# Kernel tuning notes

Measured on AMD Instinct MI355X. Metric: run time of the kernel, lower is better.

Reference implementation:

```python
import jax, jax.numpy as jnp
import numpy as np

N_NODES = 400000
N_EDGES = 800000
N_GRAPHS = 16384
IN_DIM = 78
GNN_DIMS = [128, 128, 128]
FF_DIMS = [256, 128]


def _glorot(key, shape):
    fan_in, fan_out = shape
    lim = np.sqrt(6.0 / (fan_in + fan_out))
    return jax.random.uniform(key, shape, jnp.float32, -lim, lim)


def setup_inputs() -> dict:
    key = jax.random.key(0)
    ks = jax.random.split(key, 16)
    x = jax.random.normal(ks[0], (N_NODES, IN_DIM), jnp.float32)
    edge_index = jax.random.randint(ks[1], (2, N_EDGES), 0, N_NODES, jnp.int64)
    batch = jnp.sort(jax.random.randint(ks[2], (N_NODES,), 0, N_GRAPHS, jnp.int64))
    d = dict(x=x, edge_index=edge_index, batch=batch, n_graphs=N_GRAPHS)
    dims = [IN_DIM] + GNN_DIMS
    for i in range(3):
        d[f'gW{i}'] = _glorot(ks[3 + i], (dims[i], dims[i + 1]))
        d[f'gb{i}'] = jnp.zeros((dims[i + 1],), jnp.float32)
    fdims = [GNN_DIMS[-1]] + FF_DIMS
    for i in range(2):
        d[f'fW{i}'] = _glorot(ks[8 + i], (fdims[i], fdims[i + 1]))
        d[f'fb{i}'] = jnp.zeros((fdims[i + 1],), jnp.float32)
    return d


def gcn_conv(x, src, dst, deg_isqrt, W, b, n_nodes):
    # GCNConv: linear first, then propagate with sym norm over A + I
    h = x @ W  # [N, D]
    norm = (deg_isqrt[src] * deg_isqrt[dst])[:, None]  # [E, 1]
    msg = h[src] * norm  # [E, D] gather
    out = jax.ops.segment_sum(msg, dst, num_segments=n_nodes)  # scatter-add
    # self-loop contribution: norm_ii = deg_i^-1
    out = out + h * (deg_isqrt * deg_isqrt)[:, None]
    return out + b


def reference(x, edge_index, batch, n_graphs,
              gW0, gb0, gW1, gb1, gW2, gb2,
              fW0, fb0, fW1, fb1):
    n_nodes = x.shape[0]
    src, dst = edge_index[0], edge_index[1]
    # degree of A + I on target side
    deg = 1.0 + jax.ops.segment_sum(jnp.ones((src.shape[0],), x.dtype), dst,
                                    num_segments=n_nodes)
    deg_isqrt = jax.lax.rsqrt(deg)
    for W, b in ((gW0, gb0), (gW1, gb1), (gW2, gb2)):
        x = jax.nn.relu(gcn_conv(x, src, dst, deg_isqrt, W, b, n_nodes))
    # global max pool per graph (empty segments -> 0; x >= 0 post-ReLU)
    pooled = jax.ops.segment_max(x, batch, num_segments=n_graphs)
    pooled = jnp.where(jnp.isfinite(pooled), pooled, 0.0)
    # FF head: Linear -> ReLU -> Dropout(eval: identity)
    h = jax.nn.relu(pooled @ fW0 + fb0)
    h = jax.nn.relu(h @ fW1 + fb1)
    return h
```

## Files before the change

### kernel.cpp

```cpp
#include <hip/hip_runtime.h>

#define NN 400000
#define NE 800000
#define NG 16384

typedef short bf16x8 __attribute__((ext_vector_type(8)));
typedef float f32x4 __attribute__((ext_vector_type(4)));
typedef unsigned short u16x8 __attribute__((ext_vector_type(8)));

static inline int cdiv(int a, int b) { return (a + b - 1) / b; }

__device__ inline unsigned short bf16_rne(float v) {
    unsigned u = __float_as_uint(v);
    unsigned r = u + 0x7FFFu + ((u >> 16) & 1u);
    return (unsigned short)(r >> 16);
}
__device__ inline float bf16_to_f(unsigned short h) {
    return __uint_as_float(((unsigned)h) << 16);
}
__device__ inline void split2(float v, unsigned short& hi, unsigned short& lo) {
    hi = bf16_rne(v);
    lo = bf16_rne(v - bf16_to_f(hi));
}

__global__ __launch_bounds__(256) void fill_kernel(float* __restrict__ p, float v, int n) {
    int i = blockIdx.x * blockDim.x + threadIdx.x;
    if (i < n) p[i] = v;
}

__global__ __launch_bounds__(256) void fill_int_kernel(int* __restrict__ p, int v, int n) {
    int i = blockIdx.x * blockDim.x + threadIdx.x;
    if (i < n) p[i] = v;
}

__global__ __launch_bounds__(256) void hist_kernel(const int* __restrict__ dst,
                                                   int* __restrict__ deg, int E) {
    int e = blockIdx.x * blockDim.x + threadIdx.x;
    if (e < E) atomicAdd(&deg[dst[e]], 1);
}

__global__ __launch_bounds__(256) void disq_kernel(const int* __restrict__ deg,
                                                   float* __restrict__ disq, int n) {
    int i = blockIdx.x * blockDim.x + threadIdx.x;
    if (i < n) disq[i] = rsqrtf(1.0f + (float)deg[i]);
}

#define SCAN_TPB 256
#define SCAN_EPT 8
#define SCAN_BE (SCAN_TPB * SCAN_EPT)

__global__ __launch_bounds__(SCAN_TPB) void scan_a_kernel(const int* __restrict__ in,
                                                          int* __restrict__ out,
                                                          int* __restrict__ partials, int n) {
    __shared__ int sums[SCAN_TPB];
    const int tid = threadIdx.x;
    int base = blockIdx.x * SCAN_BE + tid * SCAN_EPT;
    int v[SCAN_EPT];
    int s = 0;
#pragma unroll
    for (int i = 0; i < SCAN_EPT; ++i) {
        int idx = base + i;
        int x = (idx < n) ? in[idx] : 0;
        v[i] = s;
        s += x;
    }
    sums[tid] = s;
    __syncthreads();
    for (int off = 1; off < SCAN_TPB; off <<= 1) {
        int t = (tid >= off) ? sums[tid - off] : 0;
        __syncthreads();
        sums[tid] += t;
        __syncthreads();
    }
    int toff = (tid == 0) ? 0 : sums[tid - 1];
#pragma unroll
    for (int i = 0; i < SCAN_EPT; ++i) {
        int idx = base + i;
        if (idx < n) out[idx] = toff + v[i];
    }
    if (tid == SCAN_TPB - 1) partials[blockIdx.x] = sums[SCAN_TPB - 1];
}

__global__ void scan_b_kernel(int* __restrict__ partials, int nb) {
    if (blockIdx.x == 0 && threadIdx.x == 0) {
        int s = 0;
        for (int i = 0; i < nb; ++i) { int x = partials[i]; partials[i] = s; s += x; }
    }
}

__global__ __launch_bounds__(256) void scan_c_kernel(int* __restrict__ out,
                                                     const int* __restrict__ partials, int n) {
    int idx = blockIdx.x * blockDim.x + threadIdx.x;
    if (idx < n) out[idx] += partials[idx / SCAN_BE];
}

__global__ __launch_bounds__(256) void csr_fill_kernel(const int* __restrict__ src,
                                                       const int* __restrict__ dst,
                                                       const int* __restrict__ rowptr,
                                                       int* __restrict__ cnt,
                                                       const float* __restrict__ disq,
                                                       int2* __restrict__ csr_ent, int E) {
    int e = blockIdx.x * blockDim.x + threadIdx.x;
    if (e >= E) return;
    int d = dst[e], s = src[e];
    int pos = rowptr[d] + atomicAdd(&cnt[d], 1);
    csr_ent[pos] = make_int2(s, __float_as_int(disq[s] * disq[d]));
}

__global__ __launch_bounds__(256) void prep_w_kernel(const float* __restrict__ W,
                                                     int Ktot, int Ntot, int k0, int n0,
                                                     unsigned short* __restrict__ planeHi,
                                                     unsigned short* __restrict__ planeLo) {
    int i = blockIdx.x * blockDim.x + threadIdx.x;
    if (i >= 128 * 128) return;
    int n = i >> 7, k = i & 127;
    int gk = k0 + k, gn = n0 + n;
    float v = (gk < Ktot && gn < Ntot) ? W[(size_t)gk * Ntot + gn] : 0.0f;
    unsigned short hi, lo;
    split2(v, hi, lo);
    int elem = (n * 256 + ((2 * k) ^ ((n & 7) << 4))) >> 1;
    planeHi[elem] = hi;
    planeLo[elem] = lo;
}

__global__ __launch_bounds__(256) void xconv_kernel(const float* __restrict__ x,
                                                    unsigned short* __restrict__ xbf) {
    int t = blockIdx.x * blockDim.x + threadIdx.x;
    if (t >= NN * 24) return;
    int node = t / 24;
    int q = (t - node * 24) * 4;
    const float* xp = x + (size_t)node * 78;
    ushort4 o;
    o.x = bf16_rne((q + 0 < 78) ? xp[q + 0] : 0.0f);
    o.y = bf16_rne((q + 1 < 78) ? xp[q + 1] : 0.0f);
    o.z = bf16_rne((q + 2 < 78) ? xp[q + 2] : 0.0f);
    o.w = bf16_rne((q + 3 < 78) ? xp[q + 3] : 0.0f);
    *reinterpret_cast<ushort4*>(xbf + (size_t)node * 96 + q) = o;
}

__global__ __launch_bounds__(256) void f2bf_kernel(const float* __restrict__ in,
                                                   unsigned short* __restrict__ o, int n4) {
    int i = blockIdx.x * blockDim.x + threadIdx.x;
    if (i >= n4) return;
    float4 v = *reinterpret_cast<const float4*>(in + i * 4);
    ushort4 u;
    u.x = bf16_rne(v.x); u.y = bf16_rne(v.y); u.z = bf16_rne(v.z); u.w = bf16_rne(v.w);
    *reinterpret_cast<ushort4*>(o + i * 4) = u;
}

template <int STRIDE>
__global__ __launch_bounds__(256) void gather_kernel(const unsigned short* __restrict__ act,
                                                     const int* __restrict__ rowptr,
                                                     const int* __restrict__ deg,
                                                     const int2* __restrict__ csr_ent,
                                                     const float* __restrict__ disq,
                                                     unsigned short* __restrict__ aggHi, int n) {
    int t = blockIdx.x * blockDim.x + threadIdx.x;
    if (t >= n * 16) return;
    int node = t >> 4, q = (t & 15) * 8;
    const bool live = q < STRIDE;
    const int qc = live ? q : 0;
    int beg = rowptr[node];
    int d = deg[node];
    float si = disq[node];
    float s2 = si * si;
    u16x8 su = *reinterpret_cast<const u16x8*>(act + (size_t)node * STRIDE + qc);
    float acc[8];
#pragma unroll
    for (int i = 0; i < 8; ++i) acc[i] = bf16_to_f(su[i]) * s2;
    if (d > 0) {
        int lim = d - 1;
        int2 e[6];
#pragma unroll
        for (int j = 0; j < 6; ++j) e[j] = csr_ent[beg + (j < lim ? j : lim)];
        u16x8 u[6];
        float nr[6];
#pragma unroll
        for (int j = 0; j < 6; ++j) {
            u[j] = *reinterpret_cast<const u16x8*>(act + (size_t)e[j].x * STRIDE + qc);
            nr[j] = (j < d) ? __int_as_float(e[j].y) : 0.0f;
        }
#pragma unroll
        for (int j = 0; j < 6; ++j)
#pragma unroll
            for (int i = 0; i < 8; ++i) acc[i] = fmaf(bf16_to_f(u[j][i]), nr[j], acc[i]);
        for (int j = 6; j < d; ++j) {
            int2 ee = csr_ent[beg + j];
            float nn = __int_as_float(ee.y);
            u16x8 uu = *reinterpret_cast<const u16x8*>(act + (size_t)ee.x * STRIDE + qc);
#pragma unroll
            for (int i = 0; i < 8; ++i) acc[i] = fmaf(bf16_to_f(uu[i]), nn, acc[i]);
        }
    }
    if (live) {
        u16x8 h8;
#pragma unroll
        for (int i = 0; i < 8; ++i) h8[i] = bf16_rne(acc[i]);
        *reinterpret_cast<u16x8*>(aggHi + (size_t)node * STRIDE + q) = h8;
    }
}

template <int NKC, int AS, int MODE>
__global__ __launch_bounds__(256) void gemm_mfma_kernel(const unsigned short* __restrict__ A,
                                                        const unsigned short* __restrict__ WT,
                                                        const float* __restrict__ bias,
                                                        unsigned short* __restrict__ actout,
                                                        float* __restrict__ f32out,
                                                        const float* __restrict__ partial,
                                                        int M, int a_k0, int ostride, int ocol) {
    __shared__ unsigned short lds[2 * 128 * 128];
    const int tid = threadIdx.x;
    {
        const unsigned* s = reinterpret_cast<const unsigned*>(WT);
        unsigned* d = reinterpret_cast<unsigned*>(lds);
#pragma unroll
        for (int i = 0; i < 64; ++i) d[tid + 256 * i] = s[tid + 256 * i];
    }
    __syncthreads();

    const int w = tid >> 6, lane = tid & 63;
    const int m = lane & 15, kb = lane >> 4;
    const char* ldsHiB = reinterpret_cast<const char*>(lds);
    const char* ldsLoB = ldsHiB + 128 * 256;

    float bcol[8];
    if (MODE != 1) {
#pragma unroll
        for (int ct = 0; ct < 8; ++ct) bcol[ct] = bias[ct * 16 + m];
    }

    const int RT = 4;
    for (int rt = 0; rt < RT; ++rt) {
        int row0 = (blockIdx.x * RT + rt) * 64;
        if (row0 >= M) return;
        int arow = row0 + w * 16 + m;

        bf16x8 ah[NKC];
#pragma unroll
        for (int kc = 0; kc < NKC; ++kc)
            ah[kc] = *reinterpret_cast<const bf16x8*>(A + (size_t)arow * AS + a_k0 + kc * 32 + kb * 8);

        f32x4 acc[8];
#pragma unroll
        for (int ct = 0; ct < 8; ++ct)
#pragma unroll
            for (int r = 0; r < 4; ++r) acc[ct][r] = 0.0f;

#pragma unroll
        for (int ct = 0; ct < 8; ++ct) {
            int n = ct * 16 + m;
            int swz = (n & 7) << 4;
            int rowb = n * 256;
#pragma unroll
            for (int kc = 0; kc < NKC; ++kc) {
                int bb = rowb + ((kc * 64 + kb * 16) ^ swz);
                bf16x8 bh = *reinterpret_cast<const bf16x8*>(ldsHiB + bb);
                bf16x8 bl = *reinterpret_cast<const bf16x8*>(ldsLoB + bb);
                acc[ct] = __builtin_amdgcn_mfma_f32_16x16x32_bf16(ah[kc], bh, acc[ct], 0, 0, 0);
                acc[ct] = __builtin_amdgcn_mfma_f32_16x16x32_bf16(ah[kc], bl, acc[ct], 0, 0, 0);
            }
        }

        if (MODE == 0) {
            unsigned short* ap = actout + (size_t)(row0 + w * 16) * ostride + ocol;
#pragma unroll
            for (int ct = 0; ct < 8; ++ct)
#pragma unroll
                for (int r = 0; r < 4; ++r) {
                    float v = fmaxf(acc[ct][r] + bcol[ct], 0.0f);
                    ap[(size_t)(kb * 4 + r) * ostride + ct * 16 + m] = bf16_rne(v);
                }
        } else if (MODE == 1) {
            float* fp = f32out + (size_t)(row0 + w * 16) * 128;
#pragma unroll
            for (int ct = 0; ct < 8; ++ct)
#pragma unroll
                for (int r = 0; r < 4; ++r)
                    fp[(size_t)(kb * 4 + r) * 128 + ct * 16 + m] = acc[ct][r];
        } else {
            const float* pp = partial + (size_t)(row0 + w * 16) * 128;
            float* fp = f32out + (size_t)(row0 + w * 16) * 128;
#pragma unroll
            for (int ct = 0; ct < 8; ++ct)
#pragma unroll
                for (int r = 0; r < 4; ++r) {
                    size_t idx = (size_t)(kb * 4 + r) * 128 + ct * 16 + m;
                    float v = fmaxf(acc[ct][r] + pp[idx] + bcol[ct], 0.0f);
                    fp[idx] = v;
                }
        }
    }
}

__global__ __launch_bounds__(256) void pool_kernel(const unsigned short* __restrict__ act,
                                                   const int* __restrict__ batch,
                                                   int* __restrict__ pooled, int n) {
    int t = blockIdx.x * blockDim.x + threadIdx.x;
    int d = t & 127;
    int n0 = (t >> 7) * 8;
    if (n0 >= n) return;
    int cur = batch[n0];
    float m = fmaxf(bf16_to_f(act[(size_t)n0 * 128 + d]), 0.f);
    for (int i = 1; i < 8 && (n0 + i) < n; ++i) {
        int b = batch[n0 + i];
        float v = fmaxf(bf16_to_f(act[(size_t)(n0 + i) * 128 + d]), 0.f);
        if (b == cur) {
            m = fmaxf(m, v);
        } else {
            atomicMax(&pooled[cur * 128 + d], __float_as_int(m));
            cur = b;
            m = v;
        }
    }
    atomicMax(&pooled[cur * 128 + d], __float_as_int(m));
}

extern "C" void kernel_launch(void* const* d_in, const int* in_sizes, int n_in,
                              void* d_out, int out_size, void* d_ws, size_t ws_size,
                              hipStream_t stream) {
    const float* x    = (const float*)d_in[0];
    const int*   edge = (const int*)d_in[1];
    const int*   batch= (const int*)d_in[2];
    const float* gW0  = (const float*)d_in[4];
    const float* gb0  = (const float*)d_in[5];
    const float* gW1  = (const float*)d_in[6];
    const float* gb1  = (const float*)d_in[7];
    const float* gW2  = (const float*)d_in[8];
    const float* gb2  = (const float*)d_in[9];
    const float* fW0  = (const float*)d_in[10];
    const float* fb0  = (const float*)d_in[11];
    const float* fW1  = (const float*)d_in[12];
    const float* fb1  = (const float*)d_in[13];
    float* out = (float*)d_out;

    unsigned short* actB  = (unsigned short*)d_ws;
    unsigned short* aggHi = actB + (size_t)NN * 128;
    float* disq   = (float*)(aggHi + (size_t)NN * 128);
    float* pooled = disq + NN;
    unsigned short* pooledbf = (unsigned short*)(pooled + (size_t)NG * 128);
    unsigned short* ffhbf    = pooledbf + (size_t)NG * 128;
    int*   deg    = (int*)(ffhbf + (size_t)NG * 256);
    int*   rowptr = deg + NN;
    int2*  csr_ent = (int2*)(rowptr + NN);
    unsigned short* wt0  = (unsigned short*)(csr_ent + NE);
    unsigned short* wt1  = wt0 + 2 * 128 * 128;
    unsigned short* wt2  = wt1 + 2 * 128 * 128;
    unsigned short* wtF0a = wt2 + 2 * 128 * 128;
    unsigned short* wtF0b = wtF0a + 2 * 128 * 128;
    unsigned short* wtF1a = wtF0b + 2 * 128 * 128;
    unsigned short* wtF1b = wtF1a + 2 * 128 * 128;
    int* partials = (int*)(wtF1b + 2 * 128 * 128);
    int* cnt = (int*)pooled;
    unsigned short* xbf = actB;

    const int* src = edge;
    const int* dst = edge + NE;

    fill_int_kernel<<<cdiv(NN, 256), 256, 0, stream>>>(deg, 0, NN);
    fill_int_kernel<<<cdiv(NN, 256), 256, 0, stream>>>(cnt, 0, NN);
    hist_kernel<<<cdiv(NE, 256), 256, 0, stream>>>(dst, deg, NE);
    disq_kernel<<<cdiv(NN, 256), 256, 0, stream>>>(deg, disq, NN);
    int nsb = cdiv(NN, SCAN_BE);
    scan_a_kernel<<<nsb, SCAN_TPB, 0, stream>>>(deg, rowptr, partials, NN);
    scan_b_kernel<<<1, 64, 0, stream>>>(partials, nsb);
    scan_c_kernel<<<cdiv(NN, 256), 256, 0, stream>>>(rowptr, partials, NN);
    csr_fill_kernel<<<cdiv(NE, 256), 256, 0, stream>>>(src, dst, rowptr, cnt, disq,
                                                       csr_ent, NE);
    prep_w_kernel<<<64, 256, 0, stream>>>(gW0, 78, 128, 0, 0, wt0, wt0 + 128 * 128);
    prep_w_kernel<<<64, 256, 0, stream>>>(gW1, 128, 128, 0, 0, wt1, wt1 + 128 * 128);
    prep_w_kernel<<<64, 256, 0, stream>>>(gW2, 128, 128, 0, 0, wt2, wt2 + 128 * 128);
    prep_w_kernel<<<64, 256, 0, stream>>>(fW0, 128, 256, 0, 0,   wtF0a, wtF0a + 128 * 128);
    prep_w_kernel<<<64, 256, 0, stream>>>(fW0, 128, 256, 0, 128, wtF0b, wtF0b + 128 * 128);
    prep_w_kernel<<<64, 256, 0, stream>>>(fW1, 256, 128, 0, 0,   wtF1a, wtF1a + 128 * 128);
    prep_w_kernel<<<64, 256, 0, stream>>>(fW1, 256, 128, 128, 0, wtF1b, wtF1b + 128 * 128);
    xconv_kernel<<<cdiv(NN * 24, 256), 256, 0, stream>>>(x, xbf);

    const int gemm_blocks = cdiv(NN / 64, 4);
    const int gather_blocks = cdiv(NN * 16, 256);
    const int ff_blocks = NG / 256;

    gather_kernel<96><<<gather_blocks, 256, 0, stream>>>(xbf, rowptr, deg, csr_ent, disq,
                                                         aggHi, NN);
    gemm_mfma_kernel<3, 96, 0><<<gemm_blocks, 256, 0, stream>>>(
        aggHi, wt0, gb0, actB, nullptr, nullptr, NN, 0, 128, 0);
    gather_kernel<128><<<gather_blocks, 256, 0, stream>>>(actB, rowptr, deg, csr_ent, disq,
                                                          aggHi, NN);
    gemm_mfma_kernel<4, 128, 0><<<gemm_blocks, 256, 0, stream>>>(
        aggHi, wt1, gb1, actB, nullptr, nullptr, NN, 0, 128, 0);
    gather_kernel<128><<<gather_blocks, 256, 0, stream>>>(actB, rowptr, deg, csr_ent, disq,
                                                          aggHi, NN);
    gemm_mfma_kernel<4, 128, 0><<<gemm_blocks, 256, 0, stream>>>(
        aggHi, wt2, gb2, actB, nullptr, nullptr, NN, 0, 128, 0);

    fill_kernel<<<cdiv(NG * 128, 256), 256, 0, stream>>>(pooled, 0.0f, NG * 128);
    pool_kernel<<<cdiv(cdiv(NN, 8) * 128, 256), 256, 0, stream>>>(actB, batch, (int*)pooled, NN);
    f2bf_kernel<<<cdiv(NG * 32, 256), 256, 0, stream>>>(pooled, pooledbf, NG * 32);

    gemm_mfma_kernel<4, 128, 0><<<ff_blocks, 256, 0, stream>>>(
        pooledbf, wtF0a, fb0, ffhbf, nullptr, nullptr, NG, 0, 256, 0);
    gemm_mfma_kernel<4, 128, 0><<<ff_blocks, 256, 0, stream>>>(
        pooledbf, wtF0b, fb0 + 128, ffhbf, nullptr, nullptr, NG, 0, 256, 128);
    gemm_mfma_kernel<4, 256, 1><<<ff_blocks, 256, 0, stream>>>(
        ffhbf, wtF1a, nullptr, nullptr, pooled, nullptr, NG, 0, 128, 0);
    gemm_mfma_kernel<4, 256, 2><<<ff_blocks, 256, 0, stream>>>(
        ffhbf, wtF1b, fb1, nullptr, out, pooled, NG, 128, 128, 0);
}
```

Measured before the change: 597.8 us.

## Fuse neighbor gather with MFMA GEMM per GCN layer

```diff
diff --git a/kernel.cpp b/kernel.cpp
--- a/kernel.cpp
+++ b/kernel.cpp
@@ -148,55 +148,117 @@
     *reinterpret_cast<ushort4*>(o + i * 4) = u;
 }
 
-template <int STRIDE>
-__global__ __launch_bounds__(256) void gather_kernel(const unsigned short* __restrict__ act,
-                                                     const int* __restrict__ rowptr,
-                                                     const int* __restrict__ deg,
-                                                     const int2* __restrict__ csr_ent,
-                                                     const float* __restrict__ disq,
-                                                     unsigned short* __restrict__ aggHi, int n) {
-    int t = blockIdx.x * blockDim.x + threadIdx.x;
-    if (t >= n * 16) return;
-    int node = t >> 4, q = (t & 15) * 8;
-    const bool live = q < STRIDE;
-    const int qc = live ? q : 0;
-    int beg = rowptr[node];
-    int d = deg[node];
-    float si = disq[node];
-    float s2 = si * si;
-    u16x8 su = *reinterpret_cast<const u16x8*>(act + (size_t)node * STRIDE + qc);
-    float acc[8];
-#pragma unroll
-    for (int i = 0; i < 8; ++i) acc[i] = bf16_to_f(su[i]) * s2;
-    if (d > 0) {
-        int lim = d - 1;
+template <int NKC, int STRIDE>
+__global__ __launch_bounds__(512) void fused_layer_kernel(
+    const unsigned short* __restrict__ src_act,
+    const int* __restrict__ rowptr,
+    const int* __restrict__ deg,
+    const int2* __restrict__ csr_ent,
+    const float* __restrict__ disq,
+    const unsigned short* __restrict__ WT,
+    const float* __restrict__ bias,
+    unsigned short* __restrict__ out_act, int M) {
+    __shared__ unsigned short lds[2 * 128 * 128];
+    const int tid = threadIdx.x;
+    {
+        const unsigned* s = reinterpret_cast<const unsigned*>(WT);
+        unsigned* d = reinterpret_cast<unsigned*>(lds);
+#pragma unroll
+        for (int i = 0; i < 32; ++i) d[tid + 512 * i] = s[tid + 512 * i];
+    }
+    __syncthreads();
+
+    const int w = tid >> 6, lane = tid & 63;
+    const int m = lane & 15, kb = lane >> 4;
+    const char* ldsHiB = reinterpret_cast<const char*>(lds);
+    const char* ldsLoB = ldsHiB + 128 * 256;
+
+    float bcol[8];
+#pragma unroll
+    for (int ct = 0; ct < 8; ++ct) bcol[ct] = bias[ct * 16 + m];
+
+    const int RT = 2;
+    for (int rt = 0; rt < RT; ++rt) {
+        int row0 = (blockIdx.x * RT + rt) * 128;
+        if (row0 >= M) return;
+        int arow = row0 + w * 16 + m;
+
+        int beg = rowptr[arow];
+        int d = deg[arow];
+        float si = disq[arow];
+        float s2 = si * si;
         int2 e[6];
-#pragma unroll
-        for (int j = 0; j < 6; ++j) e[j] = csr_ent[beg + (j < lim ? j : lim)];
-        u16x8 u[6];
         float nr[6];
-#pragma unroll
-        for (int j = 0; j < 6; ++j) {
-            u[j] = *reinterpret_cast<const u16x8*>(act + (size_t)e[j].x * STRIDE + qc);
-            nr[j] = (j < d) ? __int_as_float(e[j].y) : 0.0f;
-        }
-#pragma unroll
-        for (int j = 0; j < 6; ++j)
-#pragma unroll
-            for (int i = 0; i < 8; ++i) acc[i] = fmaf(bf16_to_f(u[j][i]), nr[j], acc[i]);
-        for (int j = 6; j < d; ++j) {
-            int2 ee = csr_ent[beg + j];
-            float nn = __int_as_float(ee.y);
-            u16x8 uu = *reinterpret_cast<const u16x8*>(act + (size_t)ee.x * STRIDE + qc);
-#pragma unroll
-            for (int i = 0; i < 8; ++i) acc[i] = fmaf(bf16_to_f(uu[i]), nn, acc[i]);
-        }
-    }
-    if (live) {
-        u16x8 h8;
-#pragma unroll
-        for (int i = 0; i < 8; ++i) h8[i] = bf16_rne(acc[i]);
-        *reinterpret_cast<u16x8*>(aggHi + (size_t)node * STRIDE + q) = h8;
+        if (d > 0) {
+            int lim = d - 1;
+#pragma unroll
+            for (int j = 0; j < 6; ++j) e[j] = csr_ent[beg + (j < lim ? j : lim)];
+#pragma unroll
+            for (int j = 0; j < 6; ++j) nr[j] = (j < d) ? __int_as_float(e[j].y) : 0.0f;
+        }
+
+        bf16x8 ah[NKC];
+#pragma unroll
+        for (int kc = 0; kc < NKC; ++kc) {
+            const int qc = kc * 32 + kb * 8;
+            u16x8 su = *reinterpret_cast<const u16x8*>(src_act + (size_t)arow * STRIDE + qc);
+            float acc8[8];
+#pragma unroll
+            for (int i = 0; i < 8; ++i) acc8[i] = bf16_to_f(su[i]) * s2;
+            if (d > 0) {
+                u16x8 u[6];
+#pragma unroll
+                for (int j = 0; j < 6; ++j)
+                    u[j] = *reinterpret_cast<const u16x8*>(src_act + (size_t)e[j].x * STRIDE + qc);
+#pragma unroll
+                for (int j = 0; j < 6; ++j)
+#pragma unroll
+                    for (int i = 0; i < 8; ++i)
+                        acc8[i] = fmaf(bf16_to_f(u[j][i]), nr[j], acc8[i]);
+                for (int j = 6; j < d; ++j) {
+                    int2 ee = csr_ent[beg + j];
+                    float nn = __int_as_float(ee.y);
+                    u16x8 uu = *reinterpret_cast<const u16x8*>(src_act + (size_t)ee.x * STRIDE + qc);
+#pragma unroll
+                    for (int i = 0; i < 8; ++i)
+                        acc8[i] = fmaf(bf16_to_f(uu[i]), nn, acc8[i]);
+                }
+            }
+            bf16x8 a;
+#pragma unroll
+            for (int i = 0; i < 8; ++i) a[i] = (short)bf16_rne(acc8[i]);
+            ah[kc] = a;
+        }
+
+        f32x4 acc[8];
+#pragma unroll
+        for (int ct = 0; ct < 8; ++ct)
+#pragma unroll
+            for (int r = 0; r < 4; ++r) acc[ct][r] = 0.0f;
+
+#pragma unroll
+        for (int ct = 0; ct < 8; ++ct) {
+            int n = ct * 16 + m;
+            int swz = (n & 7) << 4;
+            int rowb = n * 256;
+#pragma unroll
+            for (int kc = 0; kc < NKC; ++kc) {
+                int bb = rowb + ((kc * 64 + kb * 16) ^ swz);
+                bf16x8 bh = *reinterpret_cast<const bf16x8*>(ldsHiB + bb);
+                bf16x8 bl = *reinterpret_cast<const bf16x8*>(ldsLoB + bb);
+                acc[ct] = __builtin_amdgcn_mfma_f32_16x16x32_bf16(ah[kc], bh, acc[ct], 0, 0, 0);
+                acc[ct] = __builtin_amdgcn_mfma_f32_16x16x32_bf16(ah[kc], bl, acc[ct], 0, 0, 0);
+            }
+        }
+
+        unsigned short* ap = out_act + (size_t)(row0 + w * 16) * 128;
+#pragma unroll
+        for (int ct = 0; ct < 8; ++ct)
+#pragma unroll
+            for (int r = 0; r < 4; ++r) {
+                float v = fmaxf(acc[ct][r] + bcol[ct], 0.0f);
+                ap[(size_t)(kb * 4 + r) * 128 + ct * 16 + m] = bf16_rne(v);
+            }
     }
 }
 
@@ -333,9 +395,10 @@
     const float* fb1  = (const float*)d_in[13];
     float* out = (float*)d_out;
 
-    unsigned short* actB  = (unsigned short*)d_ws;
-    unsigned short* aggHi = actB + (size_t)NN * 128;
-    float* disq   = (float*)(aggHi + (size_t)NN * 128);
+    unsigned short* actA = (unsigned short*)d_ws;
+    unsigned short* actC = actA + (size_t)NN * 128;
+    unsigned short* xbf  = actC + (size_t)NN * 128;
+    float* disq   = (float*)(xbf + (size_t)NN * 96);
     float* pooled = disq + NN;
     unsigned short* pooledbf = (unsigned short*)(pooled + (size_t)NG * 128);
     unsigned short* ffhbf    = pooledbf + (size_t)NG * 128;
@@ -351,7 +414,6 @@
     unsigned short* wtF1b = wtF1a + 2 * 128 * 128;
     int* partials = (int*)(wtF1b + 2 * 128 * 128);
     int* cnt = (int*)pooled;
-    unsigned short* xbf = actB;
 
     const int* src = edge;
     const int* dst = edge + NE;
@@ -375,27 +437,20 @@
     prep_w_kernel<<<64, 256, 0, stream>>>(fW1, 256, 128, 128, 0, wtF1b, wtF1b + 128 * 128);
     xconv_kernel<<<cdiv(NN * 24, 256), 256, 0, stream>>>(x, xbf);
 
-    const int gemm_blocks = cdiv(NN / 64, 4);
-    const int gather_blocks = cdiv(NN * 16, 256);
+    const int fused_blocks = cdiv(NN, 256);
+
+    fused_layer_kernel<3, 96><<<fused_blocks, 512, 0, stream>>>(
+        xbf, rowptr, deg, csr_ent, disq, wt0, gb0, actA, NN);
+    fused_layer_kernel<4, 128><<<fused_blocks, 512, 0, stream>>>(
+        actA, rowptr, deg, csr_ent, disq, wt1, gb1, actC, NN);
+    fused_layer_kernel<4, 128><<<fused_blocks, 512, 0, stream>>>(
+        actC, rowptr, deg, csr_ent, disq, wt2, gb2, actA, NN);
+
+    fill_kernel<<<cdiv(NG * 128, 256), 256, 0, stream>>>(pooled, 0.0f, NG * 128);
+    pool_kernel<<<cdiv(cdiv(NN, 8) * 128, 256), 256, 0, stream>>>(actA, batch, (int*)pooled, NN);
+    f2bf_kernel<<<cdiv(NG * 32, 256), 256, 0, stream>>>(pooled, pooledbf, NG * 32);
+
     const int ff_blocks = NG / 256;
-
-    gather_kernel<96><<<gather_blocks, 256, 0, stream>>>(xbf, rowptr, deg, csr_ent, disq,
-                                                         aggHi, NN);
-    gemm_mfma_kernel<3, 96, 0><<<gemm_blocks, 256, 0, stream>>>(
-        aggHi, wt0, gb0, actB, nullptr, nullptr, NN, 0, 128, 0);
-    gather_kernel<128><<<gather_blocks, 256, 0, stream>>>(actB, rowptr, deg, csr_ent, disq,
-                                                          aggHi, NN);
-    gemm_mfma_kernel<4, 128, 0><<<gemm_blocks, 256, 0, stream>>>(
-        aggHi, wt1, gb1, actB, nullptr, nullptr, NN, 0, 128, 0);
-    gather_kernel<128><<<gather_blocks, 256, 0, stream>>>(actB, rowptr, deg, csr_ent, disq,
-                                                          aggHi, NN);
-    gemm_mfma_kernel<4, 128, 0><<<gemm_blocks, 256, 0, stream>>>(
-        aggHi, wt2, gb2, actB, nullptr, nullptr, NN, 0, 128, 0);
-
-    fill_kernel<<<cdiv(NG * 128, 256), 256, 0, stream>>>(pooled, 0.0f, NG * 128);
-    pool_kernel<<<cdiv(cdiv(NN, 8) * 128, 256), 256, 0, stream>>>(actB, batch, (int*)pooled, NN);
-    f2bf_kernel<<<cdiv(NG * 32, 256), 256, 0, stream>>>(pooled, pooledbf, NG * 32);
-
     gemm_mfma_kernel<4, 128, 0><<<ff_blocks, 256, 0, stream>>>(
         pooledbf, wtF0a, fb0, ffhbf, nullptr, nullptr, NG, 0, 256, 0);
     gemm_mfma_kernel<4, 128, 0><<<ff_blocks, 256, 0, stream>>>(
```

New measurement: 599.0 us. Within noise of the previous version (+0.2%).
